# Optimization experiments

Hardware: AMD Instinct MI355X
Metric: run time of the kernel (lower is better)

Reference implementation:

```python
import jax, jax.numpy as jnp
import numpy as np

VOXEL = 0.1  # voxel size used in NSLoss.voxelize


def _chamfer(x, y):
    """Squared-distance chamfer terms. x: [B,N,3], y: [B,M,3].
    Returns (dist1 [B,N]: min over y for each x point, dist2 [B,M])."""
    xx = jnp.sum(x * x, axis=-1)              # [B,N]
    yy = jnp.sum(y * y, axis=-1)              # [B,M]
    zz = jnp.einsum('bnd,bmd->bnm', x, y)     # [B,N,M]
    P = xx[:, :, None] + yy[None if False else slice(None), None, :][0] if False else xx[:, :, None] + yy[:, None, :] - 2.0 * zz
    return P.min(axis=2), P.min(axis=1)


def _voxelize(coord):
    # masked_fill(nan -> inf), per-batch min over points, quantize, truncate to int
    c = jnp.where(jnp.isnan(coord), jnp.inf, coord)
    gmin = c.min(axis=1, keepdims=True)       # [B,1,3]
    grid = ((coord - gmin) / VOXEL).astype(jnp.int32)  # trunc like torch .int()
    return jax.lax.stop_gradient(grid)        # torch .int() detaches grad


def setup_inputs() -> dict:
    key = jax.random.key(0)
    k1, k2 = jax.random.split(key)
    preds = jax.random.normal(k1, (2, 8192, 3), dtype=jnp.float32)
    gts = jax.random.normal(k2, (2, 8192, 3), dtype=jnp.float32)
    return {"preds": preds, "gts": gts}


def reference(preds, gts):
    # chamfer on raw coordinates
    d1, d2 = _chamfer(preds, gts)
    loss2 = d1.mean() + d2.mean()
    # chamfer on voxelized coordinates
    pv = _voxelize(preds).astype(jnp.float32)
    gv = _voxelize(gts).astype(jnp.float32)
    d1v, d2v = _chamfer(pv, gv)
    loss1 = d1v.mean() + d2v.mean()
    return loss1 + loss2
```

## Files before the change

### kernel.cpp

```cpp
#include <hip/hip_runtime.h>
#include <math.h>

#define B 2
#define N 8192
#define PTS_STRIDE (N*3)
#define VOXEL 0.1f

#define CBLK 128
#define PBLK 1024

#define WS_ACC 16
#define WS_TICKET 17
#define WS_GMIN 20
#define WS_MINS 32
#define MINS_TOTAL 65536
#define OFF_PACK (WS_MINS + MINS_TOTAL)
#define PERG 147456
#define OFF_AFLO(g) (OFF_PACK + (g)*PERG)
#define OFF_AFHI(g) (OFF_AFLO(g) + 32768)
#define OFF_BR(g)   (OFF_AFLO(g) + 65536)
#define OFF_BV(g)   (OFF_AFLO(g) + 98304)
#define OFF_XXR(g)  (OFF_AFLO(g) + 131072)
#define OFF_XXV(g)  (OFF_AFLO(g) + 139264)

typedef __attribute__((ext_vector_type(8))) short short8;
typedef __attribute__((ext_vector_type(16))) float f16v;

union S8 { short8 v; unsigned short u[8]; };

__device__ __forceinline__ unsigned short f2bf(float f) {
    unsigned u = __float_as_uint(f);
    return (unsigned short)((u + 0x7FFFu + ((u >> 16) & 1u)) >> 16);
}
__device__ __forceinline__ float bf2f(unsigned short h) {
    return __uint_as_float(((unsigned)h) << 16);
}
__device__ __forceinline__ float voxq(float v, float g) {
    return (float)(int)((v - g) / VOXEL);
}
__device__ __forceinline__ unsigned fenc(float f) {
    const unsigned u = __float_as_uint(f);
    return (u & 0x80000000u) ? ~u : (u | 0x80000000u);
}
__device__ __forceinline__ float fdec(unsigned k) {
    const unsigned u = (k & 0x80000000u) ? (k & 0x7FFFFFFFu) : ~k;
    return __uint_as_float(u);
}

__global__ void __launch_bounds__(PBLK)
gmin_kernel(const float* __restrict__ preds,
            const float* __restrict__ gts,
            float* __restrict__ ws) {
    const int g   = blockIdx.x;
    const int arr = g >> 1;
    const int b   = g & 1;
    const float4* base4 = (const float4*)((arr ? gts : preds) + b * PTS_STRIDE);

    float m0 = INFINITY, m1 = INFINITY, m2 = INFINITY;
#pragma unroll
    for (int j = 0; j < 2; ++j) {
        const int i = j * PBLK + threadIdx.x;
        const float4 q0 = base4[i*3+0];
        const float4 q1 = base4[i*3+1];
        const float4 q2 = base4[i*3+2];
        float v;
        v = q0.x; m0 = fminf(m0, (v!=v)?INFINITY:v);
        v = q0.w; m0 = fminf(m0, (v!=v)?INFINITY:v);
        v = q1.z; m0 = fminf(m0, (v!=v)?INFINITY:v);
        v = q2.y; m0 = fminf(m0, (v!=v)?INFINITY:v);
        v = q0.y; m1 = fminf(m1, (v!=v)?INFINITY:v);
        v = q1.x; m1 = fminf(m1, (v!=v)?INFINITY:v);
        v = q1.w; m1 = fminf(m1, (v!=v)?INFINITY:v);
        v = q2.z; m1 = fminf(m1, (v!=v)?INFINITY:v);
        v = q0.z; m2 = fminf(m2, (v!=v)?INFINITY:v);
        v = q1.y; m2 = fminf(m2, (v!=v)?INFINITY:v);
        v = q2.x; m2 = fminf(m2, (v!=v)?INFINITY:v);
        v = q2.w; m2 = fminf(m2, (v!=v)?INFINITY:v);
    }
    for (int off = 32; off; off >>= 1) {
        m0 = fminf(m0, __shfl_down(m0, off));
        m1 = fminf(m1, __shfl_down(m1, off));
        m2 = fminf(m2, __shfl_down(m2, off));
    }
    __shared__ float sm[16][3];
    const int wave = threadIdx.x >> 6, lane = threadIdx.x & 63;
    if (lane == 0) { sm[wave][0] = m0; sm[wave][1] = m1; sm[wave][2] = m2; }
    __syncthreads();
    if (threadIdx.x == 0) {
        float a0 = sm[0][0], a1 = sm[0][1], a2 = sm[0][2];
        for (int w = 1; w < 16; ++w) {
            a0 = fminf(a0, sm[w][0]);
            a1 = fminf(a1, sm[w][1]);
            a2 = fminf(a2, sm[w][2]);
        }
        ws[WS_GMIN + g*3+0] = a0; ws[WS_GMIN + g*3+1] = a1; ws[WS_GMIN + g*3+2] = a2;
        if (g == 0) { ws[WS_ACC] = 0.0f; ((unsigned*)ws)[WS_TICKET] = 0u; }
    }
}

__global__ void __launch_bounds__(256)
pack_kernel(const float* __restrict__ preds,
            const float* __restrict__ gts,
            float* __restrict__ ws) {
    const int i   = blockIdx.x * 256 + threadIdx.x;
    const int g   = i >> 13;
    const int idx = i & (N-1);
    const int arr = g >> 1;
    const int b   = g & 1;
    const float* base = (arr ? gts : preds) + b * PTS_STRIDE;

    unsigned* mins = (unsigned*)ws + WS_MINS;
    mins[i] = 0xFF800000u;
    mins[i + 32768] = 0xFF800000u;

    const float g0 = ws[WS_GMIN + g*3+0];
    const float g1 = ws[WS_GMIN + g*3+1];
    const float g2 = ws[WS_GMIN + g*3+2];

    const float p0 = base[idx*3+0], p1 = base[idx*3+1], p2 = base[idx*3+2];
    const float w0 = voxq(p0, g0), w1 = voxq(p1, g1), w2 = voxq(p2, g2);
    const float rr = fmaf(p0,p0, fmaf(p1,p1, p2*p2));
    const float vv = fmaf(w0,w0, fmaf(w1,w1, w2*w2));

    const unsigned short yyh = f2bf(rr);
    const unsigned short yyl = f2bf(rr - bf2f(yyh));
    const unsigned short vvh = f2bf(vv);
    const unsigned short vvl = f2bf(vv - bf2f(vvh));
    const unsigned short ONE = 0x3F80;

    short8* AFLO = (short8*)(ws + OFF_AFLO(g));
    short8* AFHI = (short8*)(ws + OFF_AFHI(g));
    short8* BR   = (short8*)(ws + OFF_BR(g));
    short8* BV   = (short8*)(ws + OFF_BV(g));

    S8 f;
    f.u[0]=f2bf(p0); f.u[1]=f2bf(p1); f.u[2]=f2bf(p2);
    f.u[3]=yyh; f.u[4]=yyl; f.u[5]=f2bf(w0); f.u[6]=f2bf(w1); f.u[7]=f2bf(w2);
    AFLO[idx] = f.v;
    f.u[0]=vvh; f.u[1]=vvl; f.u[2]=0; f.u[3]=0; f.u[4]=0; f.u[5]=0; f.u[6]=0; f.u[7]=0;
    AFHI[idx] = f.v;
    f.u[0]=f2bf(-2.0f*p0); f.u[1]=f2bf(-2.0f*p1); f.u[2]=f2bf(-2.0f*p2);
    f.u[3]=ONE; f.u[4]=ONE; f.u[5]=0; f.u[6]=0; f.u[7]=0;
    BR[idx] = f.v;
    f.u[0]=0; f.u[1]=0; f.u[2]=0; f.u[3]=0; f.u[4]=0;
    f.u[5]=f2bf(-2.0f*w0); f.u[6]=f2bf(-2.0f*w1); f.u[7]=f2bf(-2.0f*w2);
    BV[idx] = f.v;
    ws[OFF_XXR(g) + idx] = rr;
    ws[OFF_XXV(g) + idx] = vv;
}

__global__ void __launch_bounds__(CBLK, 6)
chamfer_kernel(float* __restrict__ ws) {
    const int tid  = threadIdx.x;
    const int wave = tid >> 6, lane = tid & 63;
    const int half = lane >> 5, c32 = lane & 31;
    const int slot = blockIdx.z;
    const int dir  = slot & 1;
    const int b    = slot >> 1;
    const int gX = dir*2 + b;
    const int gY = (1-dir)*2 + b;

    const short8* Abase = (const short8*)(ws + (half ? OFF_AFHI(gY) : OFF_AFLO(gY)));
    const short8* BR = (const short8*)(ws + OFF_BR(gX));
    const short8* BV = (const short8*)(ws + OFF_BV(gX));

    const int xbase = blockIdx.x * 32;
    S8 hc;
    hc.u[0] = (c32 < 16) ? (unsigned short)0 : (unsigned short)0x3F80;
    hc.u[1] = hc.u[0];
    hc.u[2]=0; hc.u[3]=0; hc.u[4]=0; hc.u[5]=0; hc.u[6]=0; hc.u[7]=0;
    const int xcol0 = xbase + (c32 & 15);
    const short8 bf0 = (half == 0) ? ((c32 < 16) ? BR[xcol0] : BV[xcol0]) : hc.v;
    const short8 bf1 = (half == 0) ? ((c32 < 16) ? BR[xcol0+16] : BV[xcol0+16]) : hc.v;

    float mn0 = INFINITY, mn1 = INFINITY;
    const f16v Z = (f16v)(0.0f);
    const int abase0 = (blockIdx.y * 2 + wave) * 1024 + c32;

#pragma unroll 2
    for (int t = 0; t < 32; ++t) {
        const short8 a = Abase[abase0 + t*32];
        const f16v d0 = __builtin_amdgcn_mfma_f32_32x32x16_bf16(a, bf0, Z, 0, 0, 0);
        {
            float t0 = fminf(fminf(d0[0], d0[1]),  fminf(d0[2], d0[3]));
            float t1 = fminf(fminf(d0[4], d0[5]),  fminf(d0[6], d0[7]));
            float t2 = fminf(fminf(d0[8], d0[9]),  fminf(d0[10], d0[11]));
            float t3 = fminf(fminf(d0[12], d0[13]), fminf(d0[14], d0[15]));
            mn0 = fminf(mn0, fminf(fminf(t0, t1), fminf(t2, t3)));
        }
        const f16v d1 = __builtin_amdgcn_mfma_f32_32x32x16_bf16(a, bf1, Z, 0, 0, 0);
        {
            float t0 = fminf(fminf(d1[0], d1[1]),  fminf(d1[2], d1[3]));
            float t1 = fminf(fminf(d1[4], d1[5]),  fminf(d1[6], d1[7]));
            float t2 = fminf(fminf(d1[8], d1[9]),  fminf(d1[10], d1[11]));
            float t3 = fminf(fminf(d1[12], d1[13]), fminf(d1[14], d1[15]));
            mn1 = fminf(mn1, fminf(fminf(t0, t1), fminf(t2, t3)));
        }
    }

    mn0 = fminf(mn0, __shfl_xor(mn0, 32));
    mn1 = fminf(mn1, __shfl_xor(mn1, 32));

    if (half == 0) {
        unsigned* mins = (unsigned*)ws + WS_MINS;
        const int var = (c32 < 16) ? 0 : 1;
        const int e0 = ((slot*2 + var) << 13) + xcol0;
        atomicMin(&mins[e0],      fenc(mn0));
        atomicMin(&mins[e0 + 16], fenc(mn1));
    }
}

__global__ void __launch_bounds__(256)
finalize_kernel(float* __restrict__ ws, float* __restrict__ out) {
    const int g = blockIdx.x * 256 + threadIdx.x;
    const int slot = g >> 13;
    const int x    = g & (N-1);
    const int dir  = slot & 1;
    const int b    = slot >> 1;
    const int gX   = dir*2 + b;
    const unsigned* mins = (const unsigned*)ws + WS_MINS;
    float s = fdec(mins[((slot*2 + 0) << 13) + x]) + ws[OFF_XXR(gX) + x]
            + fdec(mins[((slot*2 + 1) << 13) + x]) + ws[OFF_XXV(gX) + x];
    for (int off = 32; off; off >>= 1)
        s += __shfl_down(s, off);
    __shared__ float sm[4];
    const int wave = threadIdx.x >> 6, lane = threadIdx.x & 63;
    if (lane == 0) sm[wave] = s;
    __syncthreads();
    if (threadIdx.x == 0) {
        const float bs = sm[0] + sm[1] + sm[2] + sm[3];
        atomicAdd(ws + WS_ACC, bs);
        __threadfence();
        const unsigned t = atomicAdd(&((unsigned*)ws)[WS_TICKET], 1u);
        if (t == gridDim.x - 1) {
            __threadfence();
            const float total = atomicAdd(ws + WS_ACC, 0.0f);
            out[0] = total * (1.0f / 16384.0f);
        }
    }
}

extern "C" void kernel_launch(void* const* d_in, const int* in_sizes, int n_in,
                              void* d_out, int out_size, void* d_ws, size_t ws_size,
                              hipStream_t stream) {
    const float* preds = (const float*)d_in[0];
    const float* gts   = (const float*)d_in[1];
    float* ws  = (float*)d_ws;
    float* out = (float*)d_out;

    gmin_kernel<<<dim3(4), dim3(PBLK), 0, stream>>>(preds, gts, ws);
    pack_kernel<<<dim3(128), dim3(256), 0, stream>>>(preds, gts, ws);
    chamfer_kernel<<<dim3(N/32, 4, 4), dim3(CBLK), 0, stream>>>(ws);
    finalize_kernel<<<dim3(128), dim3(256), 0, stream>>>(ws, out);
}
```

Baseline: 91.01 us.

## Fuse pack, chamfer and finalize into one cooperative kernel with grid syncs

Merges the pack, chamfer and finalize kernels into a single cooperative launch that separates the phases with grid-wide syncs, removing two launch gaps. Atomic min into an encoded buffer is replaced by plain writes of per-y-split partial minima, which finalize then reduces. This also drops the need to initialise the mins buffer. The y range is now split 4 ways instead of 8, so each wave runs a longer loop. The costs are the grid.sync overhead, fewer and larger work units, and a pack phase that runs on only 32 threads per block.

```diff
diff --git a/kernel.cpp b/kernel.cpp
--- a/kernel.cpp
+++ b/kernel.cpp
@@ -1,20 +1,22 @@
 #include <hip/hip_runtime.h>
+#include <hip/hip_cooperative_groups.h>
 #include <math.h>
+
+namespace cg = cooperative_groups;
 
 #define B 2
 #define N 8192
 #define PTS_STRIDE (N*3)
 #define VOXEL 0.1f
 
-#define CBLK 128
 #define PBLK 1024
+#define MBLK 256
+#define MGRID 1024
 
 #define WS_ACC 16
 #define WS_TICKET 17
 #define WS_GMIN 20
-#define WS_MINS 32
-#define MINS_TOTAL 65536
-#define OFF_PACK (WS_MINS + MINS_TOTAL)
+#define OFF_PACK 32
 #define PERG 147456
 #define OFF_AFLO(g) (OFF_PACK + (g)*PERG)
 #define OFF_AFHI(g) (OFF_AFLO(g) + 32768)
@@ -22,6 +24,8 @@
 #define OFF_BV(g)   (OFF_AFLO(g) + 98304)
 #define OFF_XXR(g)  (OFF_AFLO(g) + 131072)
 #define OFF_XXV(g)  (OFF_AFLO(g) + 139264)
+#define OFF_PART    (OFF_PACK + 4*PERG)
+#define PART_IDX(ys, slot, var, x) (OFF_PART + (((((ys)*4 + (slot))*2 + (var)) << 13)) + (x))
 
 typedef __attribute__((ext_vector_type(8))) short short8;
 typedef __attribute__((ext_vector_type(16))) float f16v;
@@ -37,14 +41,6 @@
 }
 __device__ __forceinline__ float voxq(float v, float g) {
     return (float)(int)((v - g) / VOXEL);
-}
-__device__ __forceinline__ unsigned fenc(float f) {
-    const unsigned u = __float_as_uint(f);
-    return (u & 0x80000000u) ? ~u : (u | 0x80000000u);
-}
-__device__ __forceinline__ float fdec(unsigned k) {
-    const unsigned u = (k & 0x80000000u) ? (k & 0x7FFFFFFFu) : ~k;
-    return __uint_as_float(u);
 }
 
 __global__ void __launch_bounds__(PBLK)
@@ -98,144 +94,152 @@
     }
 }
 
-__global__ void __launch_bounds__(256)
-pack_kernel(const float* __restrict__ preds,
+__global__ void __launch_bounds__(MBLK, 4)
+mega_kernel(const float* __restrict__ preds,
             const float* __restrict__ gts,
-            float* __restrict__ ws) {
-    const int i   = blockIdx.x * 256 + threadIdx.x;
-    const int g   = i >> 13;
-    const int idx = i & (N-1);
-    const int arr = g >> 1;
-    const int b   = g & 1;
-    const float* base = (arr ? gts : preds) + b * PTS_STRIDE;
-
-    unsigned* mins = (unsigned*)ws + WS_MINS;
-    mins[i] = 0xFF800000u;
-    mins[i + 32768] = 0xFF800000u;
-
-    const float g0 = ws[WS_GMIN + g*3+0];
-    const float g1 = ws[WS_GMIN + g*3+1];
-    const float g2 = ws[WS_GMIN + g*3+2];
-
-    const float p0 = base[idx*3+0], p1 = base[idx*3+1], p2 = base[idx*3+2];
-    const float w0 = voxq(p0, g0), w1 = voxq(p1, g1), w2 = voxq(p2, g2);
-    const float rr = fmaf(p0,p0, fmaf(p1,p1, p2*p2));
-    const float vv = fmaf(w0,w0, fmaf(w1,w1, w2*w2));
-
-    const unsigned short yyh = f2bf(rr);
-    const unsigned short yyl = f2bf(rr - bf2f(yyh));
-    const unsigned short vvh = f2bf(vv);
-    const unsigned short vvl = f2bf(vv - bf2f(vvh));
-    const unsigned short ONE = 0x3F80;
-
-    short8* AFLO = (short8*)(ws + OFF_AFLO(g));
-    short8* AFHI = (short8*)(ws + OFF_AFHI(g));
-    short8* BR   = (short8*)(ws + OFF_BR(g));
-    short8* BV   = (short8*)(ws + OFF_BV(g));
-
-    S8 f;
-    f.u[0]=f2bf(p0); f.u[1]=f2bf(p1); f.u[2]=f2bf(p2);
-    f.u[3]=yyh; f.u[4]=yyl; f.u[5]=f2bf(w0); f.u[6]=f2bf(w1); f.u[7]=f2bf(w2);
-    AFLO[idx] = f.v;
-    f.u[0]=vvh; f.u[1]=vvl; f.u[2]=0; f.u[3]=0; f.u[4]=0; f.u[5]=0; f.u[6]=0; f.u[7]=0;
-    AFHI[idx] = f.v;
-    f.u[0]=f2bf(-2.0f*p0); f.u[1]=f2bf(-2.0f*p1); f.u[2]=f2bf(-2.0f*p2);
-    f.u[3]=ONE; f.u[4]=ONE; f.u[5]=0; f.u[6]=0; f.u[7]=0;
-    BR[idx] = f.v;
-    f.u[0]=0; f.u[1]=0; f.u[2]=0; f.u[3]=0; f.u[4]=0;
-    f.u[5]=f2bf(-2.0f*w0); f.u[6]=f2bf(-2.0f*w1); f.u[7]=f2bf(-2.0f*w2);
-    BV[idx] = f.v;
-    ws[OFF_XXR(g) + idx] = rr;
-    ws[OFF_XXV(g) + idx] = vv;
-}
-
-__global__ void __launch_bounds__(CBLK, 6)
-chamfer_kernel(float* __restrict__ ws) {
-    const int tid  = threadIdx.x;
-    const int wave = tid >> 6, lane = tid & 63;
-    const int half = lane >> 5, c32 = lane & 31;
-    const int slot = blockIdx.z;
-    const int dir  = slot & 1;
-    const int b    = slot >> 1;
-    const int gX = dir*2 + b;
-    const int gY = (1-dir)*2 + b;
-
-    const short8* Abase = (const short8*)(ws + (half ? OFF_AFHI(gY) : OFF_AFLO(gY)));
-    const short8* BR = (const short8*)(ws + OFF_BR(gX));
-    const short8* BV = (const short8*)(ws + OFF_BV(gX));
-
-    const int xbase = blockIdx.x * 32;
-    S8 hc;
-    hc.u[0] = (c32 < 16) ? (unsigned short)0 : (unsigned short)0x3F80;
-    hc.u[1] = hc.u[0];
-    hc.u[2]=0; hc.u[3]=0; hc.u[4]=0; hc.u[5]=0; hc.u[6]=0; hc.u[7]=0;
-    const int xcol0 = xbase + (c32 & 15);
-    const short8 bf0 = (half == 0) ? ((c32 < 16) ? BR[xcol0] : BV[xcol0]) : hc.v;
-    const short8 bf1 = (half == 0) ? ((c32 < 16) ? BR[xcol0+16] : BV[xcol0+16]) : hc.v;
-
-    float mn0 = INFINITY, mn1 = INFINITY;
-    const f16v Z = (f16v)(0.0f);
-    const int abase0 = (blockIdx.y * 2 + wave) * 1024 + c32;
+            float* __restrict__ ws,
+            float* __restrict__ out) {
+    cg::grid_group grid = cg::this_grid();
+    const int bid = blockIdx.x;
+    const int tid = threadIdx.x;
+
+    if (tid < 32) {
+        const int g   = bid >> 8;
+        const int idx = (bid & 255) * 32 + tid;
+        const int arr = g >> 1;
+        const int b   = g & 1;
+        const float* base = (arr ? gts : preds) + b * PTS_STRIDE;
+
+        const float g0 = ws[WS_GMIN + g*3+0];
+        const float g1 = ws[WS_GMIN + g*3+1];
+        const float g2 = ws[WS_GMIN + g*3+2];
+
+        const float p0 = base[idx*3+0], p1 = base[idx*3+1], p2 = base[idx*3+2];
+        const float w0 = voxq(p0, g0), w1 = voxq(p1, g1), w2 = voxq(p2, g2);
+        const float rr = fmaf(p0,p0, fmaf(p1,p1, p2*p2));
+        const float vv = fmaf(w0,w0, fmaf(w1,w1, w2*w2));
+
+        const unsigned short yyh = f2bf(rr);
+        const unsigned short yyl = f2bf(rr - bf2f(yyh));
+        const unsigned short vvh = f2bf(vv);
+        const unsigned short vvl = f2bf(vv - bf2f(vvh));
+        const unsigned short ONE = 0x3F80;
+
+        short8* AFLO = (short8*)(ws + OFF_AFLO(g));
+        short8* AFHI = (short8*)(ws + OFF_AFHI(g));
+        short8* BR   = (short8*)(ws + OFF_BR(g));
+        short8* BV   = (short8*)(ws + OFF_BV(g));
+
+        S8 f;
+        f.u[0]=f2bf(p0); f.u[1]=f2bf(p1); f.u[2]=f2bf(p2);
+        f.u[3]=yyh; f.u[4]=yyl; f.u[5]=f2bf(w0); f.u[6]=f2bf(w1); f.u[7]=f2bf(w2);
+        AFLO[idx] = f.v;
+        f.u[0]=vvh; f.u[1]=vvl; f.u[2]=0; f.u[3]=0; f.u[4]=0; f.u[5]=0; f.u[6]=0; f.u[7]=0;
+        AFHI[idx] = f.v;
+        f.u[0]=f2bf(-2.0f*p0); f.u[1]=f2bf(-2.0f*p1); f.u[2]=f2bf(-2.0f*p2);
+        f.u[3]=ONE; f.u[4]=ONE; f.u[5]=0; f.u[6]=0; f.u[7]=0;
+        BR[idx] = f.v;
+        f.u[0]=0; f.u[1]=0; f.u[2]=0; f.u[3]=0; f.u[4]=0;
+        f.u[5]=f2bf(-2.0f*w0); f.u[6]=f2bf(-2.0f*w1); f.u[7]=f2bf(-2.0f*w2);
+        BV[idx] = f.v;
+        ws[OFF_XXR(g) + idx] = rr;
+        ws[OFF_XXV(g) + idx] = vv;
+    }
+
+    grid.sync();
+
+    {
+        const int wave = tid >> 6, lane = tid & 63;
+        const int half = lane >> 5, c32 = lane & 31;
+        const int task  = bid * 4 + wave;
+        const int xtile = task & 255;
+        const int ysub  = (task >> 8) & 3;
+        const int slot  = task >> 10;
+        const int dir   = slot & 1;
+        const int b     = slot >> 1;
+        const int gX = dir*2 + b;
+        const int gY = (1-dir)*2 + b;
+
+        const short8* Abase = (const short8*)(ws + (half ? OFF_AFHI(gY) : OFF_AFLO(gY)));
+        const short8* BR = (const short8*)(ws + OFF_BR(gX));
+        const short8* BV = (const short8*)(ws + OFF_BV(gX));
+
+        const int xbase = xtile * 32;
+        S8 hc;
+        hc.u[0] = (c32 < 16) ? (unsigned short)0 : (unsigned short)0x3F80;
+        hc.u[1] = hc.u[0];
+        hc.u[2]=0; hc.u[3]=0; hc.u[4]=0; hc.u[5]=0; hc.u[6]=0; hc.u[7]=0;
+        const int xcol0 = xbase + (c32 & 15);
+        const short8 bf0 = (half == 0) ? ((c32 < 16) ? BR[xcol0] : BV[xcol0]) : hc.v;
+        const short8 bf1 = (half == 0) ? ((c32 < 16) ? BR[xcol0+16] : BV[xcol0+16]) : hc.v;
+
+        float mn0 = INFINITY, mn1 = INFINITY;
+        const f16v Z = (f16v)(0.0f);
+        const int abase0 = ysub * 2048 + c32;
 
 #pragma unroll 2
-    for (int t = 0; t < 32; ++t) {
-        const short8 a = Abase[abase0 + t*32];
-        const f16v d0 = __builtin_amdgcn_mfma_f32_32x32x16_bf16(a, bf0, Z, 0, 0, 0);
-        {
-            float t0 = fminf(fminf(d0[0], d0[1]),  fminf(d0[2], d0[3]));
-            float t1 = fminf(fminf(d0[4], d0[5]),  fminf(d0[6], d0[7]));
-            float t2 = fminf(fminf(d0[8], d0[9]),  fminf(d0[10], d0[11]));
-            float t3 = fminf(fminf(d0[12], d0[13]), fminf(d0[14], d0[15]));
-            mn0 = fminf(mn0, fminf(fminf(t0, t1), fminf(t2, t3)));
-        }
-        const f16v d1 = __builtin_amdgcn_mfma_f32_32x32x16_bf16(a, bf1, Z, 0, 0, 0);
-        {
-            float t0 = fminf(fminf(d1[0], d1[1]),  fminf(d1[2], d1[3]));
-            float t1 = fminf(fminf(d1[4], d1[5]),  fminf(d1[6], d1[7]));
-            float t2 = fminf(fminf(d1[8], d1[9]),  fminf(d1[10], d1[11]));
-            float t3 = fminf(fminf(d1[12], d1[13]), fminf(d1[14], d1[15]));
-            mn1 = fminf(mn1, fminf(fminf(t0, t1), fminf(t2, t3)));
-        }
-    }
-
-    mn0 = fminf(mn0, __shfl_xor(mn0, 32));
-    mn1 = fminf(mn1, __shfl_xor(mn1, 32));
-
-    if (half == 0) {
-        unsigned* mins = (unsigned*)ws + WS_MINS;
-        const int var = (c32 < 16) ? 0 : 1;
-        const int e0 = ((slot*2 + var) << 13) + xcol0;
-        atomicMin(&mins[e0],      fenc(mn0));
-        atomicMin(&mins[e0 + 16], fenc(mn1));
-    }
-}
-
-__global__ void __launch_bounds__(256)
-finalize_kernel(float* __restrict__ ws, float* __restrict__ out) {
-    const int g = blockIdx.x * 256 + threadIdx.x;
-    const int slot = g >> 13;
-    const int x    = g & (N-1);
-    const int dir  = slot & 1;
-    const int b    = slot >> 1;
-    const int gX   = dir*2 + b;
-    const unsigned* mins = (const unsigned*)ws + WS_MINS;
-    float s = fdec(mins[((slot*2 + 0) << 13) + x]) + ws[OFF_XXR(gX) + x]
-            + fdec(mins[((slot*2 + 1) << 13) + x]) + ws[OFF_XXV(gX) + x];
-    for (int off = 32; off; off >>= 1)
-        s += __shfl_down(s, off);
-    __shared__ float sm[4];
-    const int wave = threadIdx.x >> 6, lane = threadIdx.x & 63;
-    if (lane == 0) sm[wave] = s;
-    __syncthreads();
-    if (threadIdx.x == 0) {
-        const float bs = sm[0] + sm[1] + sm[2] + sm[3];
-        atomicAdd(ws + WS_ACC, bs);
-        __threadfence();
-        const unsigned t = atomicAdd(&((unsigned*)ws)[WS_TICKET], 1u);
-        if (t == gridDim.x - 1) {
+        for (int t = 0; t < 64; ++t) {
+            const short8 a = Abase[abase0 + t*32];
+            const f16v d0 = __builtin_amdgcn_mfma_f32_32x32x16_bf16(a, bf0, Z, 0, 0, 0);
+            {
+                float t0 = fminf(fminf(d0[0], d0[1]),  fminf(d0[2], d0[3]));
+                float t1 = fminf(fminf(d0[4], d0[5]),  fminf(d0[6], d0[7]));
+                float t2 = fminf(fminf(d0[8], d0[9]),  fminf(d0[10], d0[11]));
+                float t3 = fminf(fminf(d0[12], d0[13]), fminf(d0[14], d0[15]));
+                mn0 = fminf(mn0, fminf(fminf(t0, t1), fminf(t2, t3)));
+            }
+            const f16v d1 = __builtin_amdgcn_mfma_f32_32x32x16_bf16(a, bf1, Z, 0, 0, 0);
+            {
+                float t0 = fminf(fminf(d1[0], d1[1]),  fminf(d1[2], d1[3]));
+                float t1 = fminf(fminf(d1[4], d1[5]),  fminf(d1[6], d1[7]));
+                float t2 = fminf(fminf(d1[8], d1[9]),  fminf(d1[10], d1[11]));
+                float t3 = fminf(fminf(d1[12], d1[13]), fminf(d1[14], d1[15]));
+                mn1 = fminf(mn1, fminf(fminf(t0, t1), fminf(t2, t3)));
+            }
+        }
+
+        mn0 = fminf(mn0, __shfl_xor(mn0, 32));
+        mn1 = fminf(mn1, __shfl_xor(mn1, 32));
+
+        if (half == 0) {
+            const int var = (c32 < 16) ? 0 : 1;
+            ws[PART_IDX(ysub, slot, var, xcol0)]      = mn0;
+            ws[PART_IDX(ysub, slot, var, xcol0 + 16)] = mn1;
+        }
+    }
+
+    grid.sync();
+
+    if (bid < 128) {
+        const int g = bid * MBLK + tid;
+        const int slot = g >> 13;
+        const int x    = g & (N-1);
+        const int dir  = slot & 1;
+        const int b    = slot >> 1;
+        const int gX   = dir*2 + b;
+        float m_r = INFINITY, m_v = INFINITY;
+#pragma unroll
+        for (int ys = 0; ys < 4; ++ys) {
+            m_r = fminf(m_r, ws[PART_IDX(ys, slot, 0, x)]);
+            m_v = fminf(m_v, ws[PART_IDX(ys, slot, 1, x)]);
+        }
+        float s = m_r + ws[OFF_XXR(gX) + x] + m_v + ws[OFF_XXV(gX) + x];
+        for (int off = 32; off; off >>= 1)
+            s += __shfl_down(s, off);
+        __shared__ float sm[4];
+        const int wave = tid >> 6, lane = tid & 63;
+        if (lane == 0) sm[wave] = s;
+        __syncthreads();
+        if (tid == 0) {
+            const float bs = sm[0] + sm[1] + sm[2] + sm[3];
+            atomicAdd(ws + WS_ACC, bs);
             __threadfence();
-            const float total = atomicAdd(ws + WS_ACC, 0.0f);
-            out[0] = total * (1.0f / 16384.0f);
+            const unsigned t = atomicAdd(&((unsigned*)ws)[WS_TICKET], 1u);
+            if (t == 127) {
+                __threadfence();
+                const float total = atomicAdd(ws + WS_ACC, 0.0f);
+                out[0] = total * (1.0f / 16384.0f);
+            }
         }
     }
 }
@@ -249,7 +253,8 @@
     float* out = (float*)d_out;
 
     gmin_kernel<<<dim3(4), dim3(PBLK), 0, stream>>>(preds, gts, ws);
-    pack_kernel<<<dim3(128), dim3(256), 0, stream>>>(preds, gts, ws);
-    chamfer_kernel<<<dim3(N/32, 4, 4), dim3(CBLK), 0, stream>>>(ws);
-    finalize_kernel<<<dim3(128), dim3(256), 0, stream>>>(ws, out);
-}
+
+    void* args[] = { (void*)&preds, (void*)&gts, (void*)&ws, (void*)&out };
+    hipLaunchCooperativeKernel((void*)mega_kernel, dim3(MGRID), dim3(MBLK),
+                               args, 0, stream);
+}
```

Measured after the change: 259.5 us. 185% more time.

## Fuse gmin and pack kernels, replace atomicMin with per-slice partial minima

Applied to the files above, without the earlier changes.

Merges the grid-min reduction and the packing step into one prep kernel, which removes a launch and the mins-buffer initialisation. The chamfer kernel now writes per-y-slice partial minima to a plain buffer instead of doing encoded atomicMin, and the finalize kernel reduces the 8 partials per point. The inner loop keeps 8 independent min accumulators to shorten the dependency chain, and occupancy is lowered to 5 to fit the extra registers. The trade-off is that the prep work now runs on only 4 blocks, and finalize reads more memory.

```diff
diff --git a/kernel.cpp b/kernel.cpp
--- a/kernel.cpp
+++ b/kernel.cpp
@@ -12,9 +12,7 @@
 #define WS_ACC 16
 #define WS_TICKET 17
 #define WS_GMIN 20
-#define WS_MINS 32
-#define MINS_TOTAL 65536
-#define OFF_PACK (WS_MINS + MINS_TOTAL)
+#define OFF_PACK 32
 #define PERG 147456
 #define OFF_AFLO(g) (OFF_PACK + (g)*PERG)
 #define OFF_AFHI(g) (OFF_AFLO(g) + 32768)
@@ -22,6 +20,8 @@
 #define OFF_BV(g)   (OFF_AFLO(g) + 98304)
 #define OFF_XXR(g)  (OFF_AFLO(g) + 131072)
 #define OFF_XXV(g)  (OFF_AFLO(g) + 139264)
+#define OFF_PART    (OFF_PACK + 4*PERG)
+#define PART_IDX(ys, slot, var, x) (OFF_PART + (((((ys)*4 + (slot))*2 + (var)) << 13)) + (x))
 
 typedef __attribute__((ext_vector_type(8))) short short8;
 typedef __attribute__((ext_vector_type(16))) float f16v;
@@ -38,23 +38,16 @@
 __device__ __forceinline__ float voxq(float v, float g) {
     return (float)(int)((v - g) / VOXEL);
 }
-__device__ __forceinline__ unsigned fenc(float f) {
-    const unsigned u = __float_as_uint(f);
-    return (u & 0x80000000u) ? ~u : (u | 0x80000000u);
-}
-__device__ __forceinline__ float fdec(unsigned k) {
-    const unsigned u = (k & 0x80000000u) ? (k & 0x7FFFFFFFu) : ~k;
-    return __uint_as_float(u);
-}
 
 __global__ void __launch_bounds__(PBLK)
-gmin_kernel(const float* __restrict__ preds,
+prep_kernel(const float* __restrict__ preds,
             const float* __restrict__ gts,
             float* __restrict__ ws) {
     const int g   = blockIdx.x;
     const int arr = g >> 1;
     const int b   = g & 1;
-    const float4* base4 = (const float4*)((arr ? gts : preds) + b * PTS_STRIDE);
+    const float* base = (arr ? gts : preds) + b * PTS_STRIDE;
+    const float4* base4 = (const float4*)base;
 
     float m0 = INFINITY, m1 = INFINITY, m2 = INFINITY;
 #pragma unroll
@@ -83,6 +76,7 @@
         m2 = fminf(m2, __shfl_down(m2, off));
     }
     __shared__ float sm[16][3];
+    __shared__ float gsh[3];
     const int wave = threadIdx.x >> 6, lane = threadIdx.x & 63;
     if (lane == 0) { sm[wave][0] = m0; sm[wave][1] = m1; sm[wave][2] = m2; }
     __syncthreads();
@@ -94,62 +88,49 @@
             a2 = fminf(a2, sm[w][2]);
         }
         ws[WS_GMIN + g*3+0] = a0; ws[WS_GMIN + g*3+1] = a1; ws[WS_GMIN + g*3+2] = a2;
+        gsh[0] = a0; gsh[1] = a1; gsh[2] = a2;
         if (g == 0) { ws[WS_ACC] = 0.0f; ((unsigned*)ws)[WS_TICKET] = 0u; }
     }
-}
-
-__global__ void __launch_bounds__(256)
-pack_kernel(const float* __restrict__ preds,
-            const float* __restrict__ gts,
-            float* __restrict__ ws) {
-    const int i   = blockIdx.x * 256 + threadIdx.x;
-    const int g   = i >> 13;
-    const int idx = i & (N-1);
-    const int arr = g >> 1;
-    const int b   = g & 1;
-    const float* base = (arr ? gts : preds) + b * PTS_STRIDE;
-
-    unsigned* mins = (unsigned*)ws + WS_MINS;
-    mins[i] = 0xFF800000u;
-    mins[i + 32768] = 0xFF800000u;
-
-    const float g0 = ws[WS_GMIN + g*3+0];
-    const float g1 = ws[WS_GMIN + g*3+1];
-    const float g2 = ws[WS_GMIN + g*3+2];
-
-    const float p0 = base[idx*3+0], p1 = base[idx*3+1], p2 = base[idx*3+2];
-    const float w0 = voxq(p0, g0), w1 = voxq(p1, g1), w2 = voxq(p2, g2);
-    const float rr = fmaf(p0,p0, fmaf(p1,p1, p2*p2));
-    const float vv = fmaf(w0,w0, fmaf(w1,w1, w2*w2));
-
-    const unsigned short yyh = f2bf(rr);
-    const unsigned short yyl = f2bf(rr - bf2f(yyh));
-    const unsigned short vvh = f2bf(vv);
-    const unsigned short vvl = f2bf(vv - bf2f(vvh));
-    const unsigned short ONE = 0x3F80;
+    __syncthreads();
+    const float g0 = gsh[0], g1 = gsh[1], g2 = gsh[2];
 
     short8* AFLO = (short8*)(ws + OFF_AFLO(g));
     short8* AFHI = (short8*)(ws + OFF_AFHI(g));
     short8* BR   = (short8*)(ws + OFF_BR(g));
     short8* BV   = (short8*)(ws + OFF_BV(g));
-
-    S8 f;
-    f.u[0]=f2bf(p0); f.u[1]=f2bf(p1); f.u[2]=f2bf(p2);
-    f.u[3]=yyh; f.u[4]=yyl; f.u[5]=f2bf(w0); f.u[6]=f2bf(w1); f.u[7]=f2bf(w2);
-    AFLO[idx] = f.v;
-    f.u[0]=vvh; f.u[1]=vvl; f.u[2]=0; f.u[3]=0; f.u[4]=0; f.u[5]=0; f.u[6]=0; f.u[7]=0;
-    AFHI[idx] = f.v;
-    f.u[0]=f2bf(-2.0f*p0); f.u[1]=f2bf(-2.0f*p1); f.u[2]=f2bf(-2.0f*p2);
-    f.u[3]=ONE; f.u[4]=ONE; f.u[5]=0; f.u[6]=0; f.u[7]=0;
-    BR[idx] = f.v;
-    f.u[0]=0; f.u[1]=0; f.u[2]=0; f.u[3]=0; f.u[4]=0;
-    f.u[5]=f2bf(-2.0f*w0); f.u[6]=f2bf(-2.0f*w1); f.u[7]=f2bf(-2.0f*w2);
-    BV[idx] = f.v;
-    ws[OFF_XXR(g) + idx] = rr;
-    ws[OFF_XXV(g) + idx] = vv;
-}
-
-__global__ void __launch_bounds__(CBLK, 6)
+    const unsigned short ONE = 0x3F80;
+
+#pragma unroll 2
+    for (int k = 0; k < 8; ++k) {
+        const int idx = k * PBLK + threadIdx.x;
+        const float p0 = base[idx*3+0], p1 = base[idx*3+1], p2 = base[idx*3+2];
+        const float w0 = voxq(p0, g0), w1 = voxq(p1, g1), w2 = voxq(p2, g2);
+        const float rr = fmaf(p0,p0, fmaf(p1,p1, p2*p2));
+        const float vv = fmaf(w0,w0, fmaf(w1,w1, w2*w2));
+
+        const unsigned short yyh = f2bf(rr);
+        const unsigned short yyl = f2bf(rr - bf2f(yyh));
+        const unsigned short vvh = f2bf(vv);
+        const unsigned short vvl = f2bf(vv - bf2f(vvh));
+
+        S8 f;
+        f.u[0]=f2bf(p0); f.u[1]=f2bf(p1); f.u[2]=f2bf(p2);
+        f.u[3]=yyh; f.u[4]=yyl; f.u[5]=f2bf(w0); f.u[6]=f2bf(w1); f.u[7]=f2bf(w2);
+        AFLO[idx] = f.v;
+        f.u[0]=vvh; f.u[1]=vvl; f.u[2]=0; f.u[3]=0; f.u[4]=0; f.u[5]=0; f.u[6]=0; f.u[7]=0;
+        AFHI[idx] = f.v;
+        f.u[0]=f2bf(-2.0f*p0); f.u[1]=f2bf(-2.0f*p1); f.u[2]=f2bf(-2.0f*p2);
+        f.u[3]=ONE; f.u[4]=ONE; f.u[5]=0; f.u[6]=0; f.u[7]=0;
+        BR[idx] = f.v;
+        f.u[0]=0; f.u[1]=0; f.u[2]=0; f.u[3]=0; f.u[4]=0;
+        f.u[5]=f2bf(-2.0f*w0); f.u[6]=f2bf(-2.0f*w1); f.u[7]=f2bf(-2.0f*w2);
+        BV[idx] = f.v;
+        ws[OFF_XXR(g) + idx] = rr;
+        ws[OFF_XXV(g) + idx] = vv;
+    }
+}
+
+__global__ void __launch_bounds__(CBLK, 5)
 chamfer_kernel(float* __restrict__ ws) {
     const int tid  = threadIdx.x;
     const int wave = tid >> 6, lane = tid & 63;
@@ -173,40 +154,38 @@
     const short8 bf0 = (half == 0) ? ((c32 < 16) ? BR[xcol0] : BV[xcol0]) : hc.v;
     const short8 bf1 = (half == 0) ? ((c32 < 16) ? BR[xcol0+16] : BV[xcol0+16]) : hc.v;
 
-    float mn0 = INFINITY, mn1 = INFINITY;
+    float mA[8], mB[8];
+#pragma unroll
+    for (int r = 0; r < 8; ++r) { mA[r] = INFINITY; mB[r] = INFINITY; }
+
     const f16v Z = (f16v)(0.0f);
-    const int abase0 = (blockIdx.y * 2 + wave) * 1024 + c32;
+    const int ysub = blockIdx.y * 2 + wave;
+    const int abase0 = ysub * 1024 + c32;
 
 #pragma unroll 2
     for (int t = 0; t < 32; ++t) {
         const short8 a = Abase[abase0 + t*32];
         const f16v d0 = __builtin_amdgcn_mfma_f32_32x32x16_bf16(a, bf0, Z, 0, 0, 0);
-        {
-            float t0 = fminf(fminf(d0[0], d0[1]),  fminf(d0[2], d0[3]));
-            float t1 = fminf(fminf(d0[4], d0[5]),  fminf(d0[6], d0[7]));
-            float t2 = fminf(fminf(d0[8], d0[9]),  fminf(d0[10], d0[11]));
-            float t3 = fminf(fminf(d0[12], d0[13]), fminf(d0[14], d0[15]));
-            mn0 = fminf(mn0, fminf(fminf(t0, t1), fminf(t2, t3)));
+        const f16v d1 = __builtin_amdgcn_mfma_f32_32x32x16_bf16(a, bf1, Z, 0, 0, 0);
+#pragma unroll
+        for (int r = 0; r < 8; ++r) {
+            mA[r] = fminf(mA[r], fminf(d0[2*r], d0[2*r+1]));
+            mB[r] = fminf(mB[r], fminf(d1[2*r], d1[2*r+1]));
         }
-        const f16v d1 = __builtin_amdgcn_mfma_f32_32x32x16_bf16(a, bf1, Z, 0, 0, 0);
-        {
-            float t0 = fminf(fminf(d1[0], d1[1]),  fminf(d1[2], d1[3]));
-            float t1 = fminf(fminf(d1[4], d1[5]),  fminf(d1[6], d1[7]));
-            float t2 = fminf(fminf(d1[8], d1[9]),  fminf(d1[10], d1[11]));
-            float t3 = fminf(fminf(d1[12], d1[13]), fminf(d1[14], d1[15]));
-            mn1 = fminf(mn1, fminf(fminf(t0, t1), fminf(t2, t3)));
-        }
-    }
+    }
+
+    float mn0 = fminf(fminf(fminf(mA[0], mA[1]), fminf(mA[2], mA[3])),
+                      fminf(fminf(mA[4], mA[5]), fminf(mA[6], mA[7])));
+    float mn1 = fminf(fminf(fminf(mB[0], mB[1]), fminf(mB[2], mB[3])),
+                      fminf(fminf(mB[4], mB[5]), fminf(mB[6], mB[7])));
 
     mn0 = fminf(mn0, __shfl_xor(mn0, 32));
     mn1 = fminf(mn1, __shfl_xor(mn1, 32));
 
     if (half == 0) {
-        unsigned* mins = (unsigned*)ws + WS_MINS;
         const int var = (c32 < 16) ? 0 : 1;
-        const int e0 = ((slot*2 + var) << 13) + xcol0;
-        atomicMin(&mins[e0],      fenc(mn0));
-        atomicMin(&mins[e0 + 16], fenc(mn1));
+        ws[PART_IDX(ysub, slot, var, xcol0)]      = mn0;
+        ws[PART_IDX(ysub, slot, var, xcol0 + 16)] = mn1;
     }
 }
 
@@ -218,9 +197,13 @@
     const int dir  = slot & 1;
     const int b    = slot >> 1;
     const int gX   = dir*2 + b;
-    const unsigned* mins = (const unsigned*)ws + WS_MINS;
-    float s = fdec(mins[((slot*2 + 0) << 13) + x]) + ws[OFF_XXR(gX) + x]
-            + fdec(mins[((slot*2 + 1) << 13) + x]) + ws[OFF_XXV(gX) + x];
+    float m_r = INFINITY, m_v = INFINITY;
+#pragma unroll
+    for (int ys = 0; ys < 8; ++ys) {
+        m_r = fminf(m_r, ws[PART_IDX(ys, slot, 0, x)]);
+        m_v = fminf(m_v, ws[PART_IDX(ys, slot, 1, x)]);
+    }
+    float s = m_r + ws[OFF_XXR(gX) + x] + m_v + ws[OFF_XXV(gX) + x];
     for (int off = 32; off; off >>= 1)
         s += __shfl_down(s, off);
     __shared__ float sm[4];
@@ -248,8 +231,7 @@
     float* ws  = (float*)d_ws;
     float* out = (float*)d_out;
 
-    gmin_kernel<<<dim3(4), dim3(PBLK), 0, stream>>>(preds, gts, ws);
-    pack_kernel<<<dim3(128), dim3(256), 0, stream>>>(preds, gts, ws);
+    prep_kernel<<<dim3(4), dim3(PBLK), 0, stream>>>(preds, gts, ws);
     chamfer_kernel<<<dim3(N/32, 4, 4), dim3(CBLK), 0, stream>>>(ws);
     finalize_kernel<<<dim3(128), dim3(256), 0, stream>>>(ws, out);
 }
```

Result: slower. 107.8 us (+18.4%).
